# Optimization experiments

Measured on AMD Instinct MI355X. Metric: run time of the kernel, lower is better.

Reference implementation:

```python
import jax, jax.numpy as jnp
import numpy as np


def _scan_dir(x, A, B, reverse):
    """First-order linear recurrence h_i = A*h_{i-1} + B*x_i along last axis (W).
    x: [Bsz, C, H, W]; A, B: [C]. reverse=True scans right-to-left but returns
    states in original index order (matching torch scan_backward)."""
    xs = jnp.moveaxis(x, -1, 0)  # [W, Bsz, C, H]
    Ab = A[None, :, None]
    Bb = B[None, :, None]
    def step(h, xi):
        h = Ab * h + Bb * xi
        return h, h
    h0 = jnp.zeros_like(xs[0])
    _, hs = jax.lax.scan(step, h0, xs, reverse=reverse)
    return jnp.moveaxis(hs, 0, -1)  # [Bsz, C, H, W]


def _conv1x1(x, W, b):
    # x: [B,Cin,H,W], W: [Cout,Cin], b: [Cout]
    return jnp.einsum('bchw,dc->bdhw', x, W) + b[None, :, None, None]


def setup_inputs() -> dict:
    key = jax.random.key(0)
    ks = jax.random.split(key, 10)
    B, C, H, W = 8, 64, 128, 128
    D = 128  # hidden_dim
    return {
        'F_in': jax.random.normal(ks[0], (B, C, H, W), dtype=jnp.float32),
        'prior': jax.random.uniform(ks[1], (B, 1, H, W), dtype=jnp.float32),
        'Wi': jax.random.normal(ks[2], (D, C), dtype=jnp.float32) * 0.05,
        'bi': jnp.zeros((D,), dtype=jnp.float32),
        'A_param': jax.random.normal(ks[3], (D,), dtype=jnp.float32),
        'B_param': jax.random.normal(ks[4], (D,), dtype=jnp.float32),
        'alpha': jnp.float32(0.1),
        'gamma': jnp.float32(0.1),
        'Wf': jax.random.normal(ks[5], (D, 4 * D), dtype=jnp.float32) * 0.05,
        'bf': jnp.zeros((D,), dtype=jnp.float32),
        'Wo': jax.random.normal(ks[6], (C, D), dtype=jnp.float32) * 0.05,
        'bo': jnp.zeros((C,), dtype=jnp.float32),
    }


def reference(F_in, prior, Wi, bi, A_param, B_param, alpha, gamma, Wf, bf, Wo, bo):
    # prior has 1 channel, repeated to C channels (prior already matches HxW)
    prior_r = jnp.broadcast_to(prior, F_in.shape)
    F_mod = F_in + alpha * prior_r
    x = _conv1x1(F_mod, Wi, bi)  # [B, D, H, W]
    A = jnp.tanh(A_param)
    Bp = B_param
    h_lr = _scan_dir(x, A, Bp, reverse=False)
    h_rl = _scan_dir(x, A, Bp, reverse=True)
    xt = jnp.swapaxes(x, 2, 3)  # scan over H axis
    h_tb = jnp.swapaxes(_scan_dir(xt, A, Bp, reverse=False), 2, 3)
    h_bt = jnp.swapaxes(_scan_dir(xt, A, Bp, reverse=True), 2, 3)
    h = jnp.concatenate([h_lr, h_rl, h_tb, h_bt], axis=1)  # [B, 4D, H, W]
    h = _conv1x1(h, Wf, bf)   # fusion -> [B, D, H, W]
    out = _conv1x1(h, Wo, bo)  # output_proj -> [B, C, H, W]
    return F_mod + gamma * out
```

## Files before the change

kernel.cpp:

```cpp
#include <hip/hip_runtime.h>
#include <hip/hip_bf16.h>

typedef unsigned int u32;
typedef unsigned short u16;
typedef float f32x2 __attribute__((ext_vector_type(2)));
typedef float f32x4 __attribute__((ext_vector_type(4)));
using bf16x8 = __attribute__((ext_vector_type(8))) short;
using f32x4v = __attribute__((ext_vector_type(4))) float;

#define DEVINL __device__ __forceinline__

constexpr int SCAN_LDS = 32768;
constexpr int XS = 132;
constexpr int LDS_X = 128 * XS * 2;

DEVINL float bf2f(u16 u) { union { u32 i; float f; } v; v.i = ((u32)u) << 16; return v.f; }
DEVINL float bf2f_lo(u32 u) { union { u32 i; float f; } v; v.i = u << 16; return v.f; }
DEVINL float bf2f_hi(u32 u) { union { u32 i; float f; } v; v.i = u & 0xffff0000u; return v.f; }
DEVINL u16 f2bf(float f) {
  __hip_bfloat16 h = __float2bfloat16(f);
  u16 r; __builtin_memcpy(&r, &h, 2); return r;
}
DEVINL u32 pack2(float a, float b) { return (u32)f2bf(a) | ((u32)f2bf(b) << 16); }

__global__ __launch_bounds__(256) void k_pre(
    const float* __restrict__ Wf, const float* __restrict__ Wo,
    const float* __restrict__ bf_, const float* __restrict__ bo,
    const float* __restrict__ A_param, const float* __restrict__ Wi,
    float* __restrict__ A_t, float* __restrict__ beff,
    u16* __restrict__ Mrow, u16* __restrict__ Wi_bf) {
  const int wg = blockIdx.x, t = threadIdx.x;
  if (wg < 128) {
    const int idx = wg * 256 + t;
    const int cout = idx >> 9;
    const int k = idx & 511;
    float s = 0.f;
    for (int d = 0; d < 128; ++d) s = fmaf(Wo[cout * 128 + d], Wf[d * 512 + k], s);
    const int dir = k >> 7, dm = k & 127;
    Mrow[(dir * 64 + cout) * 128 + dm] = f2bf(s);
  } else if (wg == 128) {
    if (t < 128) A_t[t] = tanhf(A_param[t]);
    if (t < 64) {
      float s = bo[t];
      for (int d = 0; d < 128; ++d) s = fmaf(Wo[t * 128 + d], bf_[d], s);
      beff[t] = s;
    }
  } else {
#pragma unroll
    for (int k = 0; k < 32; ++k) {
      const int i = t + k * 256;
      Wi_bf[i] = f2bf(Wi[i]);
    }
  }
}

extern __shared__ char smem[];

template <bool REV>
DEVINL void scan_local(char* buf, int dp, int chunk, f32x2 A2) {
  f32x2 h = { 0.f, 0.f };
  const u32 cb = (u32)(dp * 4);
  const int s = chunk * 32;
  u32 nx[8];
#pragma unroll
  for (int j = 0; j < 8; ++j) {
    const int i = REV ? (127 - (s + j)) : (s + j);
    nx[j] = *(const u32*)(buf + i * 128 + (cb ^ ((u32)((i & 7) << 4))));
  }
  for (int ib = 0; ib < 32; ib += 8) {
    u32 cur[8];
#pragma unroll
    for (int j = 0; j < 8; ++j) cur[j] = nx[j];
    if (ib + 8 < 32) {
#pragma unroll
      for (int j = 0; j < 8; ++j) {
        const int i2 = s + ib + 8 + j;
        const int i = REV ? (127 - i2) : i2;
        nx[j] = *(const u32*)(buf + i * 128 + (cb ^ ((u32)((i & 7) << 4))));
      }
    }
#pragma unroll
    for (int j = 0; j < 8; ++j) {
      const int i2 = s + ib + j;
      const int i = REV ? (127 - i2) : i2;
      const f32x2 xv = { bf2f_lo(cur[j]), bf2f_hi(cur[j]) };
      h = A2 * h + xv;
      *(u32*)(buf + i * 128 + (cb ^ ((u32)((i & 7) << 4)))) = pack2(h.x, h.y);
    }
  }
}

template <bool REV>
DEVINL void scan_fix(char* buf, int dp, int chunk, f32x2 A2) {
  if (chunk == 0) return;
  f32x2 q = A2;
#pragma unroll
  for (int k = 0; k < 5; ++k) q *= q;
  const u32 cb = (u32)(dp * 4);
  f32x2 C = { 0.f, 0.f };
  for (int k = 0; k < chunk; ++k) {
    const int i2 = k * 32 + 31;
    const int i = REV ? (127 - i2) : i2;
    const u32 v = *(const u32*)(buf + i * 128 + (cb ^ ((u32)((i & 7) << 4))));
    const f32x2 xv = { bf2f_lo(v), bf2f_hi(v) };
    C = C * q + xv;
  }
  f32x2 p = A2;
  const int s = chunk * 32;
  u32 nx[8];
#pragma unroll
  for (int j = 0; j < 8; ++j) {
    const int i = REV ? (127 - (s + j)) : (s + j);
    nx[j] = *(const u32*)(buf + i * 128 + (cb ^ ((u32)((i & 7) << 4))));
  }
  for (int ib = 0; ib < 32; ib += 8) {
    u32 cur[8];
#pragma unroll
    for (int j = 0; j < 8; ++j) cur[j] = nx[j];
    if (ib + 8 < 32) {
#pragma unroll
      for (int j = 0; j < 8; ++j) {
        const int i2 = s + ib + 8 + j;
        const int i = REV ? (127 - i2) : i2;
        nx[j] = *(const u32*)(buf + i * 128 + (cb ^ ((u32)((i & 7) << 4))));
      }
    }
#pragma unroll
    for (int j = 0; j < 8; ++j) {
      const int i2 = s + ib + j;
      const int i = REV ? (127 - i2) : i2;
      const f32x2 xv = { bf2f_lo(cur[j]), bf2f_hi(cur[j]) };
      const f32x2 hv = p * C + xv;
      *(u32*)(buf + i * 128 + (cb ^ ((u32)((i & 7) << 4)))) = pack2(hv.x, hv.y);
      p *= A2;
    }
  }
}

DEVINL void run_scans(char* bufA, char* bufB, int t, int e, const float* __restrict__ A_t) {
  const int dp = t & 31, chunk = (t >> 5) & 3, dir = t >> 7;
  const f32x2 a = *(const f32x2*)(A_t + e * 64 + dp * 2);
  char* sb = dir ? bufB : bufA;
  if (dir == 0) scan_local<false>(sb, dp, chunk, a);
  else          scan_local<true >(sb, dp, chunk, a);
  __syncthreads();
  if (dir == 0) scan_fix<false>(sb, dp, chunk, a);
  else          scan_fix<true >(sb, dp, chunk, a);
}

DEVINL void combine64(const char* buf, const u16* __restrict__ Mrow, int dir, int e,
                      int lane, int wv, f32x4v (&acc2)[4][2]) {
  const int l15 = lane & 15, kg = lane >> 4;
#pragma unroll
  for (int ks = 0; ks < 2; ++ks) {
    bf16x8 afr[4], bfr[2];
#pragma unroll
    for (int ct = 0; ct < 4; ++ct)
      afr[ct] = *(const bf16x8*)(Mrow + ((size_t)dir * 64 + ct * 16 + l15) * 128 + e * 64 + ks * 32 + kg * 8);
#pragma unroll
    for (int pt = 0; pt < 2; ++pt) {
      const int row = wv * 32 + pt * 16 + l15;
      bfr[pt] = *(const bf16x8*)(buf + row * 128 + ((u32)(ks * 64 + kg * 16) ^ ((u32)((row & 7) << 4))));
    }
#pragma unroll
    for (int ct = 0; ct < 4; ++ct)
#pragma unroll
      for (int pt = 0; pt < 2; ++pt)
        acc2[ct][pt] = __builtin_amdgcn_mfma_f32_16x16x32_bf16(bfr[pt], afr[ct], acc2[ct][pt], 0, 0, 0);
  }
}

DEVINL void acc_to_outs(const f32x4v (&acc2)[4][2], int lane, int wv, char* buf) {
  const int l15 = lane & 15, kg = lane >> 4;
#pragma unroll
  for (int ct = 0; ct < 4; ++ct)
#pragma unroll
    for (int pt = 0; pt < 2; ++pt) {
      const int c = ct * 16 + l15;
      const int pos = wv * 32 + pt * 16 + kg * 4;
      *(f32x4v*)(buf + c * 512 + ((u32)(pos * 4) ^ ((u32)((c & 7) << 4)))) = acc2[ct][pt];
    }
}

DEVINL void outs_to_global(const char* buf, u16* __restrict__ og, int t) {
#pragma unroll
  for (int j = 0; j < 16; ++j) {
    const int i = t + j * 256;
    const int c = i >> 6, p2 = (i & 63) * 2;
    const f32x2 v = *(const f32x2*)(buf + c * 512 + ((u32)(p2 * 4) ^ ((u32)((c & 7) << 4))));
    *(u32*)(og + c * 128 + p2) = pack2(v.x, v.y);
  }
}

__global__ __launch_bounds__(256, 5) void k_A(
    const float* __restrict__ F_in, const float* __restrict__ prior,
    const u16* __restrict__ Wi_bf, const float* __restrict__ bi,
    const float* __restrict__ Bp, const float* __restrict__ alpha_p,
    const float* __restrict__ A_t, const u16* __restrict__ Mrow,
    u16* __restrict__ x2, u16* __restrict__ Shp) {
  char* bufA = smem;
  char* bufB = smem + 16384;

  const int t = threadIdx.x;
  const int lane = t & 63, wv = t >> 6, l15 = lane & 15, kg = lane >> 4;
  const int bid = blockIdx.x;
  const int b = bid >> 8, h = (bid >> 1) & 127, e = bid & 1;

  {
    const int w = t & 127, ch = t >> 7;
    const float alpha = alpha_p[0];
    const float pv = prior[(b * 128 + h) * 128 + w];
    const float* Fb = F_in + ((size_t)b * 64 + ch * 32) * 16384 + h * 128 + w;
    const u32 sw = (u32)((w & 7) << 4);
    char* rowp = bufA + w * 128;
#pragma unroll
    for (int q = 0; q < 4; ++q) {
      float fv[8];
#pragma unroll
      for (int j = 0; j < 8; ++j) fv[j] = fmaf(alpha, pv, Fb[(q * 8 + j) * 16384]);
      uint4 pk;
      pk.x = pack2(fv[0], fv[1]); pk.y = pack2(fv[2], fv[3]);
      pk.z = pack2(fv[4], fv[5]); pk.w = pack2(fv[6], fv[7]);
      *(uint4*)(rowp + ((u32)(ch * 64 + q * 16) ^ sw)) = pk;
    }
  }
  __syncthreads();

  bf16x8 bF[2][2];
#pragma unroll
  for (int wj = 0; wj < 2; ++wj)
#pragma unroll
    for (int ks = 0; ks < 2; ++ks) {
      const int row = wv * 32 + wj * 16 + l15;
      bF[wj][ks] = *(const bf16x8*)(bufA + row * 128 + ((u32)(ks * 64 + kg * 16) ^ ((u32)((row & 7) << 4))));
    }
  __syncthreads();

  {
    f32x4v acc[4][2];
#pragma unroll
    for (int dt = 0; dt < 4; ++dt) {
      const f32x4 bv = *(const f32x4*)(bi + e * 64 + dt * 16 + kg * 4);
      const f32x4v bvv = { bv.x, bv.y, bv.z, bv.w };
#pragma unroll
      for (int wj = 0; wj < 2; ++wj) acc[dt][wj] = bvv;
    }
#pragma unroll
    for (int ks = 0; ks < 2; ++ks)
#pragma unroll
      for (int dt = 0; dt < 4; ++dt) {
        const bf16x8 aWi = *(const bf16x8*)(Wi_bf + (e * 64 + dt * 16 + l15) * 64 + ks * 32 + kg * 8);
        acc[dt][0] = __builtin_amdgcn_mfma_f32_16x16x32_bf16(aWi, bF[0][ks], acc[dt][0], 0, 0, 0);
        acc[dt][1] = __builtin_amdgcn_mfma_f32_16x16x32_bf16(aWi, bF[1][ks], acc[dt][1], 0, 0, 0);
      }
#pragma unroll
    for (int dt = 0; dt < 4; ++dt) {
      const f32x4 B4 = *(const f32x4*)(Bp + e * 64 + dt * 16 + kg * 4);
      const f32x4v B4v = { B4.x, B4.y, B4.z, B4.w };
#pragma unroll
      for (int wj = 0; wj < 2; ++wj) {
        const f32x4v sv = acc[dt][wj] * B4v;
        const int w = wv * 32 + wj * 16 + l15;
        const int dl = dt * 16 + kg * 4;
        uint2 pk;
        pk.x = pack2(sv[0], sv[1]);
        pk.y = pack2(sv[2], sv[3]);
        const u32 col = (u32)(dl * 2) ^ ((u32)((w & 7) << 4));
        *(uint2*)(bufA + w * 128 + col) = pk;
        *(uint2*)(bufB + w * 128 + col) = pk;
      }
    }
  }
  __syncthreads();

  {
    u16* xg = x2 + (size_t)bid * 8192;
#pragma unroll
    for (int j = 0; j < 4; ++j) {
      const int idx = t + j * 256;
      const int row = idx >> 3, q = idx & 7;
      const uint4 v = *(const uint4*)(bufA + row * 128 + ((u32)(q * 16) ^ ((u32)((row & 7) << 4))));
      *(uint4*)(xg + row * 64 + q * 8) = v;
    }
  }
  __syncthreads();

  run_scans(bufA, bufB, t, e, A_t);
  __syncthreads();

  f32x4v acc2[4][2];
#pragma unroll
  for (int i = 0; i < 4; ++i)
#pragma unroll
    for (int j = 0; j < 2; ++j) acc2[i][j] = (f32x4v)0.f;
  combine64(bufA, Mrow, 0, e, lane, wv, acc2);
  combine64(bufB, Mrow, 1, e, lane, wv, acc2);
  __syncthreads();

  acc_to_outs(acc2, lane, wv, smem);
  __syncthreads();

  outs_to_global(smem, Shp + (size_t)bid * 8192, t);
}

__global__ __launch_bounds__(256, 5) void k_B(
    const u16* __restrict__ x2,
    const float* __restrict__ A_t, const u16* __restrict__ Mrow,
    u16* __restrict__ Svp) {
  char* bufA = smem;
  char* bufB = smem + 16384;
  const int t = threadIdx.x;
  const int lane = t & 63, wv = t >> 6;
  const int bid = blockIdx.x;
  const int b = bid >> 8, w = (bid >> 1) & 127, e = bid & 1;

#pragma unroll
  for (int j = 0; j < 4; ++j) {
    const int idx = t + j * 256;
    const int hh = idx >> 3, q = idx & 7;
    const uint4 v = *(const uint4*)(x2 + ((size_t)((b * 128 + hh) * 2 + e)) * 8192 + w * 64 + q * 8);
    const u32 col = (u32)(q * 16) ^ ((u32)((hh & 7) << 4));
    *(uint4*)(bufA + hh * 128 + col) = v;
    *(uint4*)(bufB + hh * 128 + col) = v;
  }
  __syncthreads();

  run_scans(bufA, bufB, t, e, A_t);
  __syncthreads();

  f32x4v acc2[4][2];
#pragma unroll
  for (int i = 0; i < 4; ++i)
#pragma unroll
    for (int j = 0; j < 2; ++j) acc2[i][j] = (f32x4v)0.f;
  combine64(bufA, Mrow, 2, e, lane, wv, acc2);
  combine64(bufB, Mrow, 3, e, lane, wv, acc2);
  __syncthreads();

  acc_to_outs(acc2, lane, wv, smem);
  __syncthreads();

  outs_to_global(smem, Svp + (size_t)bid * 8192, t);
}

__global__ __launch_bounds__(256) void k_final(
    const float* __restrict__ F_in, const float* __restrict__ prior,
    const float* __restrict__ alpha_p, const float* __restrict__ gamma_p,
    const float* __restrict__ beff, const u16* __restrict__ Svp,
    const u16* __restrict__ Shp, float* __restrict__ out) {
  u16* Xu = (u16*)smem;
  const int t = threadIdx.x;
  const int bid = blockIdx.x, b = bid >> 6, c = bid & 63;
  const size_t base = (size_t)bid * 16384;

  for (int i = t; i < 2048; i += 256) {
    const int w = i >> 4, q = i & 15;
    const u16* s0 = Svp + ((size_t)((b * 128 + w) * 2)) * 8192 + c * 128 + q * 8;
    const uint4 a4 = *(const uint4*)(s0);
    const uint4 b4 = *(const uint4*)(s0 + 8192);
    const u16* ap = (const u16*)&a4;
    const u16* bp = (const u16*)&b4;
    u32* dst = (u32*)(Xu + w * 132 + q * 8);
#pragma unroll
    for (int k = 0; k < 4; ++k) {
      const float lo = bf2f(ap[k * 2]) + bf2f(bp[k * 2]);
      const float hi = bf2f(ap[k * 2 + 1]) + bf2f(bp[k * 2 + 1]);
      dst[k] = pack2(lo, hi);
    }
  }
  __syncthreads();
  const float alpha = alpha_p[0], gamma = gamma_p[0];
  const float be = beff[c];
  for (int i = t; i < 2048; i += 256) {
    const int hh = i >> 4, w8 = (i & 15) * 8;
    const size_t off = base + hh * 128 + w8;
    const u16* sh0 = Shp + ((size_t)((b * 128 + hh) * 2)) * 8192 + c * 128 + w8;
    const uint4 g0 = *(const uint4*)(sh0);
    const uint4 g1 = *(const uint4*)(sh0 + 8192);
    const u16* p0 = (const u16*)&g0;
    const u16* p1 = (const u16*)&g1;
    const float* Fp = F_in + off;
    float* Op = out + off;
    const float* Pp = prior + (b * 128 + hh) * 128 + w8;
#pragma unroll
    for (int q = 0; q < 8; ++q) {
      const float sv = bf2f(Xu[(w8 + q) * 132 + hh]);
      Op[q] = Fp[q] + alpha * Pp[q] + gamma * (bf2f(p0[q]) + bf2f(p1[q]) + sv + be);
    }
  }
}

extern "C" void kernel_launch(void* const* d_in, const int* in_sizes, int n_in,
                              void* d_out, int out_size, void* d_ws, size_t ws_size,
                              hipStream_t stream) {
  const float* F_in   = (const float*)d_in[0];
  const float* prior  = (const float*)d_in[1];
  const float* Wi     = (const float*)d_in[2];
  const float* bi     = (const float*)d_in[3];
  const float* A_par  = (const float*)d_in[4];
  const float* B_par  = (const float*)d_in[5];
  const float* alpha  = (const float*)d_in[6];
  const float* gamma  = (const float*)d_in[7];
  const float* Wf     = (const float*)d_in[8];
  const float* bf_    = (const float*)d_in[9];
  const float* Wo     = (const float*)d_in[10];
  const float* bo     = (const float*)d_in[11];
  float* out = (float*)d_out;

  char* ws = (char*)d_ws;
  float* A_t   = (float*)ws;
  float* beff  = (float*)(ws + 512);
  u16*   Mrow  = (u16*)(ws + 1024);
  u16*   Wi_bf = (u16*)(ws + 66560);
  u16*   x2    = (u16*)(ws + 82944);
  u16*   Shp   = (u16*)(ws + 82944 + 33554432);
  u16*   Svp   = (u16*)(ws + 82944 + 67108864);

  hipFuncSetAttribute((const void*)k_A, hipFuncAttributeMaxDynamicSharedMemorySize, SCAN_LDS);
  hipFuncSetAttribute((const void*)k_B, hipFuncAttributeMaxDynamicSharedMemorySize, SCAN_LDS);

  k_pre  <<<130, 256, 0, stream>>>(Wf, Wo, bf_, bo, A_par, Wi, A_t, beff, Mrow, Wi_bf);
  k_A    <<<2048, 256, SCAN_LDS, stream>>>(F_in, prior, Wi_bf, bi, B_par, alpha, A_t, Mrow, x2, Shp);
  k_B    <<<2048, 256, SCAN_LDS, stream>>>(x2, A_t, Mrow, Svp);
  k_final<<<512, 256, LDS_X, stream>>>(F_in, prior, alpha, gamma, beff, Svp, Shp, out);
}
```

Baseline: 100.5 us.

## Merge k_A channel halves into one 512-thread block per row

k_A now processes all 128 hidden channels for one (b,h) row in a single 512-thread block instead of splitting channels across two 256-thread blocks. This removes the duplicated F_in/prior loads and lets the combine step reduce over all 128 channels inside the block, so Shp stores one partial per row instead of two and k_final reads half as much Shp data. The cost is double the LDS per block (64 KB) and a different x2 layout, which k_B now reads with adjusted indexing; fewer resident blocks per CU may reduce occupancy.

```diff
diff --git a/kernel.cpp b/kernel.cpp
--- a/kernel.cpp
+++ b/kernel.cpp
@@ -10,7 +10,8 @@
 
 #define DEVINL __device__ __forceinline__
 
-constexpr int SCAN_LDS = 32768;
+constexpr int LDS_A = 65536;
+constexpr int LDS_B = 32768;
 constexpr int XS = 132;
 constexpr int LDS_X = 128 * XS * 2;
 
@@ -56,7 +57,7 @@
 
 extern __shared__ char smem[];
 
-template <bool REV>
+template <bool REV, int ROWB>
 DEVINL void scan_local(char* buf, int dp, int chunk, f32x2 A2) {
   f32x2 h = { 0.f, 0.f };
   const u32 cb = (u32)(dp * 4);
@@ -65,7 +66,7 @@
 #pragma unroll
   for (int j = 0; j < 8; ++j) {
     const int i = REV ? (127 - (s + j)) : (s + j);
-    nx[j] = *(const u32*)(buf + i * 128 + (cb ^ ((u32)((i & 7) << 4))));
+    nx[j] = *(const u32*)(buf + i * ROWB + (cb ^ ((u32)((i & 7) << 4))));
   }
   for (int ib = 0; ib < 32; ib += 8) {
     u32 cur[8];
@@ -76,7 +77,7 @@
       for (int j = 0; j < 8; ++j) {
         const int i2 = s + ib + 8 + j;
         const int i = REV ? (127 - i2) : i2;
-        nx[j] = *(const u32*)(buf + i * 128 + (cb ^ ((u32)((i & 7) << 4))));
+        nx[j] = *(const u32*)(buf + i * ROWB + (cb ^ ((u32)((i & 7) << 4))));
       }
     }
 #pragma unroll
@@ -85,12 +86,12 @@
       const int i = REV ? (127 - i2) : i2;
       const f32x2 xv = { bf2f_lo(cur[j]), bf2f_hi(cur[j]) };
       h = A2 * h + xv;
-      *(u32*)(buf + i * 128 + (cb ^ ((u32)((i & 7) << 4)))) = pack2(h.x, h.y);
-    }
-  }
-}
-
-template <bool REV>
+      *(u32*)(buf + i * ROWB + (cb ^ ((u32)((i & 7) << 4)))) = pack2(h.x, h.y);
+    }
+  }
+}
+
+template <bool REV, int ROWB>
 DEVINL void scan_fix(char* buf, int dp, int chunk, f32x2 A2) {
   if (chunk == 0) return;
   f32x2 q = A2;
@@ -101,7 +102,7 @@
   for (int k = 0; k < chunk; ++k) {
     const int i2 = k * 32 + 31;
     const int i = REV ? (127 - i2) : i2;
-    const u32 v = *(const u32*)(buf + i * 128 + (cb ^ ((u32)((i & 7) << 4))));
+    const u32 v = *(const u32*)(buf + i * ROWB + (cb ^ ((u32)((i & 7) << 4))));
     const f32x2 xv = { bf2f_lo(v), bf2f_hi(v) };
     C = C * q + xv;
   }
@@ -111,7 +112,7 @@
 #pragma unroll
   for (int j = 0; j < 8; ++j) {
     const int i = REV ? (127 - (s + j)) : (s + j);
-    nx[j] = *(const u32*)(buf + i * 128 + (cb ^ ((u32)((i & 7) << 4))));
+    nx[j] = *(const u32*)(buf + i * ROWB + (cb ^ ((u32)((i & 7) << 4))));
   }
   for (int ib = 0; ib < 32; ib += 8) {
     u32 cur[8];
@@ -122,7 +123,7 @@
       for (int j = 0; j < 8; ++j) {
         const int i2 = s + ib + 8 + j;
         const int i = REV ? (127 - i2) : i2;
-        nx[j] = *(const u32*)(buf + i * 128 + (cb ^ ((u32)((i & 7) << 4))));
+        nx[j] = *(const u32*)(buf + i * ROWB + (cb ^ ((u32)((i & 7) << 4))));
       }
     }
 #pragma unroll
@@ -131,97 +132,43 @@
       const int i = REV ? (127 - i2) : i2;
       const f32x2 xv = { bf2f_lo(cur[j]), bf2f_hi(cur[j]) };
       const f32x2 hv = p * C + xv;
-      *(u32*)(buf + i * 128 + (cb ^ ((u32)((i & 7) << 4)))) = pack2(hv.x, hv.y);
+      *(u32*)(buf + i * ROWB + (cb ^ ((u32)((i & 7) << 4)))) = pack2(hv.x, hv.y);
       p *= A2;
     }
   }
 }
 
-DEVINL void run_scans(char* bufA, char* bufB, int t, int e, const float* __restrict__ A_t) {
-  const int dp = t & 31, chunk = (t >> 5) & 3, dir = t >> 7;
-  const f32x2 a = *(const f32x2*)(A_t + e * 64 + dp * 2);
-  char* sb = dir ? bufB : bufA;
-  if (dir == 0) scan_local<false>(sb, dp, chunk, a);
-  else          scan_local<true >(sb, dp, chunk, a);
-  __syncthreads();
-  if (dir == 0) scan_fix<false>(sb, dp, chunk, a);
-  else          scan_fix<true >(sb, dp, chunk, a);
-}
-
-DEVINL void combine64(const char* buf, const u16* __restrict__ Mrow, int dir, int e,
-                      int lane, int wv, f32x4v (&acc2)[4][2]) {
-  const int l15 = lane & 15, kg = lane >> 4;
-#pragma unroll
-  for (int ks = 0; ks < 2; ++ks) {
-    bf16x8 afr[4], bfr[2];
-#pragma unroll
-    for (int ct = 0; ct < 4; ++ct)
-      afr[ct] = *(const bf16x8*)(Mrow + ((size_t)dir * 64 + ct * 16 + l15) * 128 + e * 64 + ks * 32 + kg * 8);
-#pragma unroll
-    for (int pt = 0; pt < 2; ++pt) {
-      const int row = wv * 32 + pt * 16 + l15;
-      bfr[pt] = *(const bf16x8*)(buf + row * 128 + ((u32)(ks * 64 + kg * 16) ^ ((u32)((row & 7) << 4))));
-    }
-#pragma unroll
-    for (int ct = 0; ct < 4; ++ct)
-#pragma unroll
-      for (int pt = 0; pt < 2; ++pt)
-        acc2[ct][pt] = __builtin_amdgcn_mfma_f32_16x16x32_bf16(bfr[pt], afr[ct], acc2[ct][pt], 0, 0, 0);
-  }
-}
-
-DEVINL void acc_to_outs(const f32x4v (&acc2)[4][2], int lane, int wv, char* buf) {
-  const int l15 = lane & 15, kg = lane >> 4;
-#pragma unroll
-  for (int ct = 0; ct < 4; ++ct)
-#pragma unroll
-    for (int pt = 0; pt < 2; ++pt) {
-      const int c = ct * 16 + l15;
-      const int pos = wv * 32 + pt * 16 + kg * 4;
-      *(f32x4v*)(buf + c * 512 + ((u32)(pos * 4) ^ ((u32)((c & 7) << 4)))) = acc2[ct][pt];
-    }
-}
-
-DEVINL void outs_to_global(const char* buf, u16* __restrict__ og, int t) {
-#pragma unroll
-  for (int j = 0; j < 16; ++j) {
-    const int i = t + j * 256;
-    const int c = i >> 6, p2 = (i & 63) * 2;
-    const f32x2 v = *(const f32x2*)(buf + c * 512 + ((u32)(p2 * 4) ^ ((u32)((c & 7) << 4))));
-    *(u32*)(og + c * 128 + p2) = pack2(v.x, v.y);
-  }
-}
-
-__global__ __launch_bounds__(256, 5) void k_A(
+__global__ __launch_bounds__(512, 4) void k_A(
     const float* __restrict__ F_in, const float* __restrict__ prior,
     const u16* __restrict__ Wi_bf, const float* __restrict__ bi,
     const float* __restrict__ Bp, const float* __restrict__ alpha_p,
     const float* __restrict__ A_t, const u16* __restrict__ Mrow,
     u16* __restrict__ x2, u16* __restrict__ Shp) {
   char* bufA = smem;
-  char* bufB = smem + 16384;
+  char* bufB = smem + 32768;
 
   const int t = threadIdx.x;
-  const int lane = t & 63, wv = t >> 6, l15 = lane & 15, kg = lane >> 4;
-  const int bid = blockIdx.x;
-  const int b = bid >> 8, h = (bid >> 1) & 127, e = bid & 1;
+  const int lane = t & 63, wv = t >> 6;
+  const int l15 = lane & 15, kg = lane >> 4;
+  const int bid = blockIdx.x, b = bid >> 7, h = bid & 127;
+  const int wq = wv & 3, eh = wv >> 2;
 
   {
     const int w = t & 127, ch = t >> 7;
     const float alpha = alpha_p[0];
     const float pv = prior[(b * 128 + h) * 128 + w];
-    const float* Fb = F_in + ((size_t)b * 64 + ch * 32) * 16384 + h * 128 + w;
+    const float* Fb = F_in + ((size_t)b * 64 + ch * 16) * 16384 + h * 128 + w;
     const u32 sw = (u32)((w & 7) << 4);
-    char* rowp = bufA + w * 128;
-#pragma unroll
-    for (int q = 0; q < 4; ++q) {
+    char* rowp = bufA + w * 256;
+#pragma unroll
+    for (int q = 0; q < 2; ++q) {
       float fv[8];
 #pragma unroll
       for (int j = 0; j < 8; ++j) fv[j] = fmaf(alpha, pv, Fb[(q * 8 + j) * 16384]);
       uint4 pk;
       pk.x = pack2(fv[0], fv[1]); pk.y = pack2(fv[2], fv[3]);
       pk.z = pack2(fv[4], fv[5]); pk.w = pack2(fv[6], fv[7]);
-      *(uint4*)(rowp + ((u32)(ch * 64 + q * 16) ^ sw)) = pk;
+      *(uint4*)(rowp + ((u32)(ch * 32 + q * 16) ^ sw)) = pk;
     }
   }
   __syncthreads();
@@ -231,8 +178,8 @@
   for (int wj = 0; wj < 2; ++wj)
 #pragma unroll
     for (int ks = 0; ks < 2; ++ks) {
-      const int row = wv * 32 + wj * 16 + l15;
-      bF[wj][ks] = *(const bf16x8*)(bufA + row * 128 + ((u32)(ks * 64 + kg * 16) ^ ((u32)((row & 7) << 4))));
+      const int row = wq * 32 + wj * 16 + l15;
+      bF[wj][ks] = *(const bf16x8*)(bufA + row * 256 + ((u32)(ks * 64 + kg * 16) ^ ((u32)((row & 7) << 4))));
     }
   __syncthreads();
 
@@ -240,7 +187,7 @@
     f32x4v acc[4][2];
 #pragma unroll
     for (int dt = 0; dt < 4; ++dt) {
-      const f32x4 bv = *(const f32x4*)(bi + e * 64 + dt * 16 + kg * 4);
+      const f32x4 bv = *(const f32x4*)(bi + eh * 64 + dt * 16 + kg * 4);
       const f32x4v bvv = { bv.x, bv.y, bv.z, bv.w };
 #pragma unroll
       for (int wj = 0; wj < 2; ++wj) acc[dt][wj] = bvv;
@@ -249,58 +196,102 @@
     for (int ks = 0; ks < 2; ++ks)
 #pragma unroll
       for (int dt = 0; dt < 4; ++dt) {
-        const bf16x8 aWi = *(const bf16x8*)(Wi_bf + (e * 64 + dt * 16 + l15) * 64 + ks * 32 + kg * 8);
+        const bf16x8 aWi = *(const bf16x8*)(Wi_bf + (eh * 64 + dt * 16 + l15) * 64 + ks * 32 + kg * 8);
         acc[dt][0] = __builtin_amdgcn_mfma_f32_16x16x32_bf16(aWi, bF[0][ks], acc[dt][0], 0, 0, 0);
         acc[dt][1] = __builtin_amdgcn_mfma_f32_16x16x32_bf16(aWi, bF[1][ks], acc[dt][1], 0, 0, 0);
       }
 #pragma unroll
     for (int dt = 0; dt < 4; ++dt) {
-      const f32x4 B4 = *(const f32x4*)(Bp + e * 64 + dt * 16 + kg * 4);
+      const f32x4 B4 = *(const f32x4*)(Bp + eh * 64 + dt * 16 + kg * 4);
       const f32x4v B4v = { B4.x, B4.y, B4.z, B4.w };
 #pragma unroll
       for (int wj = 0; wj < 2; ++wj) {
         const f32x4v sv = acc[dt][wj] * B4v;
-        const int w = wv * 32 + wj * 16 + l15;
-        const int dl = dt * 16 + kg * 4;
+        const int w = wq * 32 + wj * 16 + l15;
+        const int dl = eh * 64 + dt * 16 + kg * 4;
         uint2 pk;
         pk.x = pack2(sv[0], sv[1]);
         pk.y = pack2(sv[2], sv[3]);
         const u32 col = (u32)(dl * 2) ^ ((u32)((w & 7) << 4));
-        *(uint2*)(bufA + w * 128 + col) = pk;
-        *(uint2*)(bufB + w * 128 + col) = pk;
-      }
-    }
-  }
-  __syncthreads();
-
-  {
-    u16* xg = x2 + (size_t)bid * 8192;
+        *(uint2*)(bufA + w * 256 + col) = pk;
+        *(uint2*)(bufB + w * 256 + col) = pk;
+      }
+    }
+  }
+  __syncthreads();
+
+  {
+    u16* xg = x2 + (size_t)bid * 16384;
 #pragma unroll
     for (int j = 0; j < 4; ++j) {
-      const int idx = t + j * 256;
-      const int row = idx >> 3, q = idx & 7;
-      const uint4 v = *(const uint4*)(bufA + row * 128 + ((u32)(q * 16) ^ ((u32)((row & 7) << 4))));
-      *(uint4*)(xg + row * 64 + q * 8) = v;
-    }
-  }
-  __syncthreads();
-
-  run_scans(bufA, bufB, t, e, A_t);
-  __syncthreads();
-
-  f32x4v acc2[4][2];
-#pragma unroll
-  for (int i = 0; i < 4; ++i)
+      const int idx = t + j * 512;
+      const int row = idx >> 4, q = idx & 15;
+      const uint4 v = *(const uint4*)(bufA + row * 256 + ((u32)(q * 16) ^ ((u32)((row & 7) << 4))));
+      *(uint4*)(xg + row * 128 + q * 8) = v;
+    }
+  }
+  __syncthreads();
+
+  {
+    const int sub = t & 255, dp = sub & 63, chunk = sub >> 6, dir = t >> 8;
+    const f32x2 a = *(const f32x2*)(A_t + dp * 2);
+    char* sb = dir ? bufB : bufA;
+    if (dir == 0) scan_local<false, 256>(sb, dp, chunk, a);
+    else          scan_local<true , 256>(sb, dp, chunk, a);
+    __syncthreads();
+    if (dir == 0) scan_fix<false, 256>(sb, dp, chunk, a);
+    else          scan_fix<true , 256>(sb, dp, chunk, a);
+  }
+  __syncthreads();
+
+  f32x4v acc2[2][2];
+#pragma unroll
+  for (int i = 0; i < 2; ++i)
 #pragma unroll
     for (int j = 0; j < 2; ++j) acc2[i][j] = (f32x4v)0.f;
-  combine64(bufA, Mrow, 0, e, lane, wv, acc2);
-  combine64(bufB, Mrow, 1, e, lane, wv, acc2);
-  __syncthreads();
-
-  acc_to_outs(acc2, lane, wv, smem);
-  __syncthreads();
-
-  outs_to_global(smem, Shp + (size_t)bid * 8192, t);
+#pragma unroll
+  for (int dir = 0; dir < 2; ++dir) {
+    const char* buf = dir ? bufB : bufA;
+#pragma unroll
+    for (int ks = 0; ks < 4; ++ks) {
+      bf16x8 afr[2], bfr[2];
+#pragma unroll
+      for (int ct = 0; ct < 2; ++ct)
+        afr[ct] = *(const bf16x8*)(Mrow + ((size_t)dir * 64 + eh * 32 + ct * 16 + l15) * 128 + ks * 32 + kg * 8);
+#pragma unroll
+      for (int pt = 0; pt < 2; ++pt) {
+        const int row = wq * 32 + pt * 16 + l15;
+        bfr[pt] = *(const bf16x8*)(buf + row * 256 + ((u32)(ks * 64 + kg * 16) ^ ((u32)((row & 7) << 4))));
+      }
+#pragma unroll
+      for (int ct = 0; ct < 2; ++ct)
+#pragma unroll
+        for (int pt = 0; pt < 2; ++pt)
+          acc2[ct][pt] = __builtin_amdgcn_mfma_f32_16x16x32_bf16(bfr[pt], afr[ct], acc2[ct][pt], 0, 0, 0);
+    }
+  }
+  __syncthreads();
+
+#pragma unroll
+  for (int ct = 0; ct < 2; ++ct)
+#pragma unroll
+    for (int pt = 0; pt < 2; ++pt) {
+      const int c = eh * 32 + ct * 16 + l15;
+      const int pos = wq * 32 + pt * 16 + kg * 4;
+      *(f32x4v*)(smem + c * 512 + ((u32)(pos * 4) ^ ((u32)((c & 7) << 4)))) = acc2[ct][pt];
+    }
+  __syncthreads();
+
+  {
+    u16* og = Shp + (size_t)bid * 8192;
+#pragma unroll
+    for (int j = 0; j < 8; ++j) {
+      const int i = t + j * 512;
+      const int c = i >> 6, p2 = (i & 63) * 2;
+      const f32x2 v = *(const f32x2*)(smem + c * 512 + ((u32)(p2 * 4) ^ ((u32)((c & 7) << 4))));
+      *(u32*)(og + c * 128 + p2) = pack2(v.x, v.y);
+    }
+  }
 }
 
 __global__ __launch_bounds__(256, 5) void k_B(
@@ -310,7 +301,7 @@
   char* bufA = smem;
   char* bufB = smem + 16384;
   const int t = threadIdx.x;
-  const int lane = t & 63, wv = t >> 6;
+  const int lane = t & 63, wv = t >> 6, l15 = lane & 15, kg = lane >> 4;
   const int bid = blockIdx.x;
   const int b = bid >> 8, w = (bid >> 1) & 127, e = bid & 1;
 
@@ -318,14 +309,23 @@
   for (int j = 0; j < 4; ++j) {
     const int idx = t + j * 256;
     const int hh = idx >> 3, q = idx & 7;
-    const uint4 v = *(const uint4*)(x2 + ((size_t)((b * 128 + hh) * 2 + e)) * 8192 + w * 64 + q * 8);
+    const uint4 v = *(const uint4*)(x2 + ((size_t)(b * 128 + hh) * 128 + w) * 128 + e * 64 + q * 8);
     const u32 col = (u32)(q * 16) ^ ((u32)((hh & 7) << 4));
     *(uint4*)(bufA + hh * 128 + col) = v;
     *(uint4*)(bufB + hh * 128 + col) = v;
   }
   __syncthreads();
 
-  run_scans(bufA, bufB, t, e, A_t);
+  {
+    const int dp = t & 31, chunk = (t >> 5) & 3, dir = t >> 7;
+    const f32x2 a = *(const f32x2*)(A_t + e * 64 + dp * 2);
+    char* sb = dir ? bufB : bufA;
+    if (dir == 0) scan_local<false, 128>(sb, dp, chunk, a);
+    else          scan_local<true , 128>(sb, dp, chunk, a);
+    __syncthreads();
+    if (dir == 0) scan_fix<false, 128>(sb, dp, chunk, a);
+    else          scan_fix<true , 128>(sb, dp, chunk, a);
+  }
   __syncthreads();
 
   f32x4v acc2[4][2];
@@ -333,14 +333,49 @@
   for (int i = 0; i < 4; ++i)
 #pragma unroll
     for (int j = 0; j < 2; ++j) acc2[i][j] = (f32x4v)0.f;
-  combine64(bufA, Mrow, 2, e, lane, wv, acc2);
-  combine64(bufB, Mrow, 3, e, lane, wv, acc2);
-  __syncthreads();
-
-  acc_to_outs(acc2, lane, wv, smem);
-  __syncthreads();
-
-  outs_to_global(smem, Svp + (size_t)bid * 8192, t);
+#pragma unroll
+  for (int dir = 0; dir < 2; ++dir) {
+    const char* buf = dir ? bufB : bufA;
+#pragma unroll
+    for (int ks = 0; ks < 2; ++ks) {
+      bf16x8 afr[4], bfr[2];
+#pragma unroll
+      for (int ct = 0; ct < 4; ++ct)
+        afr[ct] = *(const bf16x8*)(Mrow + ((size_t)(dir + 2) * 64 + ct * 16 + l15) * 128 + e * 64 + ks * 32 + kg * 8);
+#pragma unroll
+      for (int pt = 0; pt < 2; ++pt) {
+        const int row = wv * 32 + pt * 16 + l15;
+        bfr[pt] = *(const bf16x8*)(buf + row * 128 + ((u32)(ks * 64 + kg * 16) ^ ((u32)((row & 7) << 4))));
+      }
+#pragma unroll
+      for (int ct = 0; ct < 4; ++ct)
+#pragma unroll
+        for (int pt = 0; pt < 2; ++pt)
+          acc2[ct][pt] = __builtin_amdgcn_mfma_f32_16x16x32_bf16(bfr[pt], afr[ct], acc2[ct][pt], 0, 0, 0);
+    }
+  }
+  __syncthreads();
+
+#pragma unroll
+  for (int ct = 0; ct < 4; ++ct)
+#pragma unroll
+    for (int pt = 0; pt < 2; ++pt) {
+      const int c = ct * 16 + l15;
+      const int pos = wv * 32 + pt * 16 + kg * 4;
+      *(f32x4v*)(smem + c * 512 + ((u32)(pos * 4) ^ ((u32)((c & 7) << 4)))) = acc2[ct][pt];
+    }
+  __syncthreads();
+
+  {
+    u16* og = Svp + (size_t)bid * 8192;
+#pragma unroll
+    for (int j = 0; j < 16; ++j) {
+      const int i = t + j * 256;
+      const int c = i >> 6, p2 = (i & 63) * 2;
+      const f32x2 v = *(const f32x2*)(smem + c * 512 + ((u32)(p2 * 4) ^ ((u32)((c & 7) << 4))));
+      *(u32*)(og + c * 128 + p2) = pack2(v.x, v.y);
+    }
+  }
 }
 
 __global__ __launch_bounds__(256) void k_final(
@@ -374,18 +409,16 @@
   for (int i = t; i < 2048; i += 256) {
     const int hh = i >> 4, w8 = (i & 15) * 8;
     const size_t off = base + hh * 128 + w8;
-    const u16* sh0 = Shp + ((size_t)((b * 128 + hh) * 2)) * 8192 + c * 128 + w8;
+    const u16* sh0 = Shp + (size_t)(b * 128 + hh) * 8192 + c * 128 + w8;
     const uint4 g0 = *(const uint4*)(sh0);
-    const uint4 g1 = *(const uint4*)(sh0 + 8192);
     const u16* p0 = (const u16*)&g0;
-    const u16* p1 = (const u16*)&g1;
     const float* Fp = F_in + off;
     float* Op = out + off;
     const float* Pp = prior + (b * 128 + hh) * 128 + w8;
 #pragma unroll
     for (int q = 0; q < 8; ++q) {
       const float sv = bf2f(Xu[(w8 + q) * 132 + hh]);
-      Op[q] = Fp[q] + alpha * Pp[q] + gamma * (bf2f(p0[q]) + bf2f(p1[q]) + sv + be);
+      Op[q] = Fp[q] + alpha * Pp[q] + gamma * (bf2f(p0[q]) + sv + be);
     }
   }
 }
@@ -416,11 +449,11 @@
   u16*   Shp   = (u16*)(ws + 82944 + 33554432);
   u16*   Svp   = (u16*)(ws + 82944 + 67108864);
 
-  hipFuncSetAttribute((const void*)k_A, hipFuncAttributeMaxDynamicSharedMemorySize, SCAN_LDS);
-  hipFuncSetAttribute((const void*)k_B, hipFuncAttributeMaxDynamicSharedMemorySize, SCAN_LDS);
+  hipFuncSetAttribute((const void*)k_A, hipFuncAttributeMaxDynamicSharedMemorySize, LDS_A);
+  hipFuncSetAttribute((const void*)k_B, hipFuncAttributeMaxDynamicSharedMemorySize, LDS_B);
 
   k_pre  <<<130, 256, 0, stream>>>(Wf, Wo, bf_, bo, A_par, Wi, A_t, beff, Mrow, Wi_bf);
-  k_A    <<<2048, 256, SCAN_LDS, stream>>>(F_in, prior, Wi_bf, bi, B_par, alpha, A_t, Mrow, x2, Shp);
-  k_B    <<<2048, 256, SCAN_LDS, stream>>>(x2, A_t, Mrow, Svp);
+  k_A    <<<1024, 512, LDS_A, stream>>>(F_in, prior, Wi_bf, bi, B_par, alpha, A_t, Mrow, x2, Shp);
+  k_B    <<<2048, 256, LDS_B, stream>>>(x2, A_t, Mrow, Svp);
   k_final<<<512, 256, LDS_X, stream>>>(F_in, prior, alpha, gamma, beff, Svp, Shp, out);
 }
```

New measurement: 96.86 us. -3.7%, faster.
